# Performance work log

Hardware: AMD Instinct MI355X
Metric: run time of the kernel (lower is better)

Reference implementation:

```python
import jax, jax.numpy as jnp
import numpy as np

N, E = 50000, 800000
IN, HID, H, L, OUT = 128, 64, 2, 2, 40
EPS_SM = 1e-16  # PyG softmax eps
EPS_LN = 1e-5


def setup_inputs() -> dict:
    key = jax.random.key(0)
    ks = jax.random.split(key, 18)
    s = 0.05
    rn = lambda k, sh: jax.random.normal(k, sh, jnp.float32) * s
    return {
        "x": jax.random.normal(ks[0], (N, IN), jnp.float32),
        "edge_index": jax.random.randint(ks[1], (2, E), 0, N, jnp.int64),
        "emb_w": rn(ks[2], (IN, HID)),
        "emb_b": jnp.zeros((HID,), jnp.float32),
        "Wq": rn(ks[3], (L, HID, H * HID)),
        "Wk": rn(ks[4], (L, HID, H * HID)),
        "Wv": rn(ks[5], (L, HID, H * HID)),
        "Wout": rn(ks[6], (L, H * HID, HID)),
        "bout": jnp.zeros((L, HID), jnp.float32),
        "ln_g": jnp.ones((L, HID), jnp.float32),
        "ln_b": jnp.zeros((L, HID), jnp.float32),
        "W1": rn(ks[7], (L, HID, HID)),
        "b1": jnp.zeros((L, HID), jnp.float32),
        "W2": rn(ks[8], (L, HID, HID)),
        "b2": jnp.zeros((L, HID), jnp.float32),
        "out_w": rn(ks[9], (HID, OUT)),
        "out_b": jnp.zeros((OUT,), jnp.float32),
    }


def _layernorm(x, g, b):
    mu = jnp.mean(x, axis=-1, keepdims=True)
    var = jnp.mean(jnp.square(x - mu), axis=-1, keepdims=True)
    return (x - mu) * jax.lax.rsqrt(var + EPS_LN) * g + b


def _gt_layer(h, src, dst, Wq, Wk, Wv, Wout, bout):
    n = h.shape[0]
    Q = (h @ Wq).reshape(n, H, HID)
    K = (h @ Wk).reshape(n, H, HID)
    V = (h @ Wv).reshape(n, H, HID)
    # per-edge gather: q at target i, k/v at source j
    alpha = jnp.sum(Q[dst] * K[src], axis=-1) / np.sqrt(HID)  # [E, H]
    # segment softmax keyed by target node
    amax = jax.ops.segment_max(alpha, dst, num_segments=n)    # [N, H]
    a = jnp.exp(alpha - amax[dst])
    denom = jax.ops.segment_sum(a, dst, num_segments=n)
    a = a / (denom[dst] + EPS_SM)
    msg = V[src] * a[..., None]                               # [E, H, HID]
    aggr = jax.ops.segment_sum(msg, dst, num_segments=n)      # [N, H, HID]
    return aggr.reshape(n, H * HID) @ Wout + bout


def reference(x, edge_index, emb_w, emb_b, Wq, Wk, Wv, Wout, bout,
              ln_g, ln_b, W1, b1, W2, b2, out_w, out_b):
    src, dst = edge_index[0], edge_index[1]
    h = x @ emb_w + emb_b
    for l in range(L):
        res = h
        h = _gt_layer(h, src, dst, Wq[l], Wk[l], Wv[l], Wout[l], bout[l])
        h = _layernorm(h + res, ln_g[l], ln_b[l])
        h = h + (jax.nn.relu(h @ W1[l] + b1[l]) @ W2[l] + b2[l])
    return jax.nn.log_softmax(h @ out_w + out_b, axis=-1)
```

## Files before the change

### kernel.cpp

```cpp
#include <hip/hip_runtime.h>
#include <math.h>

#define DIN 128
#define HID 64
#define BKTSH 7
#define NBKTCAP 512
#define CAPC 2560

typedef _Float16 h2 __attribute__((ext_vector_type(2)));
typedef _Float16 f16x8 __attribute__((ext_vector_type(8)));
typedef float f32x4 __attribute__((ext_vector_type(4)));
typedef float f32x2 __attribute__((ext_vector_type(2)));

__device__ inline unsigned short f2h(float f) {
  return __builtin_bit_cast(unsigned short, (_Float16)f);
}
__device__ inline h2 bch2(unsigned int u) { return __builtin_bit_cast(h2, u); }
__device__ inline unsigned int h2u(h2 x) { return __builtin_bit_cast(unsigned int, x); }
__device__ inline unsigned int pkrtz(float a, float b) {
  return __builtin_bit_cast(unsigned int, __builtin_amdgcn_cvt_pkrtz(a, b));
}
__device__ inline f16x8 bcf16x8(uint4 u) { return __builtin_bit_cast(f16x8, u); }


__global__ __launch_bounds__(256) void k_bktA(const int* __restrict__ dst,
                                              int* __restrict__ bhist,
                                              int nblkA, int E, int nbkt) {
  __shared__ int hist[NBKTCAP];
  int tid = threadIdx.x;
  for (int i = tid; i < nbkt; i += 256) hist[i] = 0;
  __syncthreads();
#pragma unroll
  for (int i = 0; i < 16; ++i) {
    int e = blockIdx.x * 4096 + i * 256 + tid;
    if (e < E) atomicAdd(&hist[dst[e] >> BKTSH], 1);
  }
  __syncthreads();
  for (int i = tid; i < nbkt; i += 256) bhist[i * nblkA + blockIdx.x] = hist[i];
}

__global__ __launch_bounds__(256) void k_bktScan1(int* __restrict__ bhist,
                                                  int* __restrict__ btot,
                                                  int nblkA, int nbkt) {
  int wv = threadIdx.x >> 6, lane = threadIdx.x & 63;
  int b = blockIdx.x * 4 + wv;
  if (b >= nbkt) return;
  int* rowp = bhist + (size_t)b * nblkA;
  int carry = 0;
  for (int base = 0; base < nblkA; base += 64) {
    int i = base + lane;
    int v = (i < nblkA) ? rowp[i] : 0;
    int incl = v;
#pragma unroll
    for (int d = 1; d < 64; d <<= 1) {
      int t = __shfl_up(incl, d, 64);
      if (lane >= d) incl += t;
    }
    if (i < nblkA) rowp[i] = carry + incl - v;
    carry += __shfl(incl, 63, 64);
  }
  if (lane == 0) btot[b] = carry;
}

__global__ __launch_bounds__(512) void k_bktScan2(const int* __restrict__ btot,
                                                  int* __restrict__ bktBase,
                                                  int* __restrict__ rowp,
                                                  int nbkt, int E, int n) {
  __shared__ int sc[512];
  int b = threadIdx.x;
  int s = (b < nbkt) ? btot[b] : 0;
  sc[b] = s;
  __syncthreads();
  for (int d = 1; d < 512; d <<= 1) {
    int v = (b >= d) ? sc[b - d] : 0;
    __syncthreads();
    sc[b] += v;
    __syncthreads();
  }
  if (b < nbkt) bktBase[b] = sc[b] - s;
  if (b == 0) {
    bktBase[nbkt] = E;
    rowp[n] = E;
  }
}

__global__ __launch_bounds__(256) void k_bktB(const int* __restrict__ src,
                                              const int* __restrict__ dst,
                                              const int* __restrict__ bpos,
                                              const int* __restrict__ bktBase,
                                              int2* __restrict__ ebuf,
                                              int nblkA, int E, int nbkt) {
  __shared__ int cur[NBKTCAP];
  int tid = threadIdx.x;
  for (int i = tid; i < nbkt; i += 256)
    cur[i] = bpos[i * nblkA + blockIdx.x] + bktBase[i];
  __syncthreads();
#pragma unroll
  for (int i = 0; i < 16; ++i) {
    int e = blockIdx.x * 4096 + i * 256 + tid;
    if (e < E) {
      int d = dst[e];
      int pos = atomicAdd(&cur[d >> BKTSH], 1);
      ebuf[pos] = make_int2(src[e], d);
    }
  }
}

__global__ __launch_bounds__(256) void k_bktC(const int2* __restrict__ ebuf,
                                              const int* __restrict__ bktBase,
                                              int* __restrict__ rowp,
                                              int* __restrict__ deg,
                                              int* __restrict__ srcs, int n) {
  __shared__ int2 rec[CAPC];
  __shared__ int outv[CAPC];
  __shared__ int hist[128];
  __shared__ int sc[128];
  __shared__ int cur2[128];
  int b = blockIdx.x;
  int tid = threadIdx.x;
  int s0 = bktBase[b], s1 = bktBase[b + 1];
  int cnt = s1 - s0;
  int nodeBase = b << BKTSH;
  if (tid < 128) hist[tid] = 0;
  __syncthreads();
  bool fast = (cnt <= CAPC);
  if (fast) {
    for (int i = tid; i < cnt; i += 256) {
      int2 r = ebuf[s0 + i];
      rec[i] = r;
      atomicAdd(&hist[r.y & 127], 1);
    }
  } else {
    for (int i = tid; i < cnt; i += 256) atomicAdd(&hist[ebuf[s0 + i].y & 127], 1);
  }
  __syncthreads();
  if (tid < 128) sc[tid] = hist[tid];
  __syncthreads();
  for (int d = 1; d < 128; d <<= 1) {
    int v = (tid < 128 && tid >= d) ? sc[tid - d] : 0;
    __syncthreads();
    if (tid < 128) sc[tid] += v;
    __syncthreads();
  }
  if (tid < 128) {
    int excl = sc[tid] - hist[tid];
    int node = nodeBase + tid;
    if (node < n) {
      rowp[node] = s0 + excl;
      deg[node] = hist[tid];
    }
    cur2[tid] = excl;
  }
  __syncthreads();
  if (fast) {
    for (int i = tid; i < cnt; i += 256) {
      int2 r = rec[i];
      int pos = atomicAdd(&cur2[r.y & 127], 1);
      outv[pos] = r.x;
    }
    __syncthreads();
    for (int i = tid; i < cnt; i += 256) srcs[s0 + i] = outv[i];
  } else {
    for (int i = tid; i < cnt; i += 256) {
      int2 r = ebuf[s0 + i];
      int pos = atomicAdd(&cur2[r.y & 127], 1);
      srcs[s0 + pos] = r.x;
    }
  }
}

__global__ __launch_bounds__(256) void k_dhist(const int* __restrict__ cnt,
                                               int* __restrict__ bhist, int n) {
  __shared__ int hist[64];
  int tid = threadIdx.x;
  if (tid < 64) hist[tid] = 0;
  __syncthreads();
  int base = blockIdx.x * 2048 + tid * 8;
#pragma unroll
  for (int i = 0; i < 8; ++i) {
    int idx = base + i;
    if (idx < n) atomicAdd(&hist[min(cnt[idx], 63)], 1);
  }
  __syncthreads();
  if (tid < 64) bhist[blockIdx.x * 64 + tid] = hist[tid];
}

__global__ void k_dscan2(const int* __restrict__ bhist, int* __restrict__ bbase,
                         int nblk) {
  int b = threadIdx.x;
  int tot = 0;
  for (int blk = 0; blk < nblk; ++blk) tot += bhist[blk * 64 + b];
  int incl = tot;
#pragma unroll
  for (int d = 1; d < 64; d <<= 1) {
    int t = __shfl_up(incl, d, 64);
    if (b >= d) incl += t;
  }
  int run = incl - tot;
  for (int blk = 0; blk < nblk; ++blk) {
    bbase[blk * 64 + b] = run;
    run += bhist[blk * 64 + b];
  }
}

__global__ __launch_bounds__(256) void k_dscat2(const int* __restrict__ cnt,
                                                const int* __restrict__ bbase,
                                                int* __restrict__ perm, int n) {
  __shared__ int cur[64];
  int tid = threadIdx.x;
  if (tid < 64) cur[tid] = bbase[blockIdx.x * 64 + tid];
  __syncthreads();
  int base = blockIdx.x * 2048 + tid * 8;
#pragma unroll
  for (int i = 0; i < 8; ++i) {
    int idx = base + i;
    if (idx < n) {
      int pos = atomicAdd(&cur[min(cnt[idx], 63)], 1);
      perm[pos] = idx;
    }
  }
}

__global__ __launch_bounds__(256) void k_wpack(
    const float* __restrict__ Wq, const float* __restrict__ Wk,
    const float* __restrict__ Wv, const float* __restrict__ Wout,
    const float* __restrict__ W1, const float* __restrict__ W2,
    uint4* __restrict__ P) {
  int t = blockIdx.x * 256 + threadIdx.x;
  if (t >= 10240) return;
  int layer = t / 5120;
  int r = t - layer * 5120;
  const float* W;
  int idx, nkk, ld, base;
  float scale = 1.f;
  if (r < 1024) {
    W = Wq + layer * 64 * 128; idx = r; nkk = 2; ld = 128;
    scale = 0.125f * 1.44269504089f; base = 0;
  } else if (r < 2048) {
    W = Wk + layer * 64 * 128; idx = r - 1024; nkk = 2; ld = 128; base = 1024;
  } else if (r < 3072) {
    W = Wv + layer * 64 * 128; idx = r - 2048; nkk = 2; ld = 128; base = 2048;
  } else if (r < 4096) {
    W = Wout + layer * 128 * 64; idx = r - 3072; nkk = 4; ld = 64; base = 3072;
  } else if (r < 4608) {
    W = W1 + layer * 64 * 64; idx = r - 4096; nkk = 2; ld = 64; base = 4096;
  } else {
    W = W2 + layer * 64 * 64; idx = r - 4608; nkk = 2; ld = 64; base = 4608;
  }
  int lane = idx & 63;
  int g = idx >> 6;
  int ct = g / nkk, kk = g - ct * nkk;
  int lc = lane & 15, lg = lane >> 4;
  unsigned short o[8];
#pragma unroll
  for (int i = 0; i < 8; ++i)
    o[i] = f2h(W[(kk * 32 + lg * 8 + i) * ld + ct * 16 + lc] * scale);
  P[layer * 5120 + base + idx] = *(const uint4*)o;
}

__global__ __launch_bounds__(256) void k_wpack2(const float* __restrict__ emb_w,
                                                const float* __restrict__ out_w,
                                                uint4* __restrict__ P) {
  int t = blockIdx.x * 256 + threadIdx.x;
  if (t >= 1408) return;
  int lane, ct, kk, lc, lg;
  unsigned short o[8];
  if (t < 1024) {
    int idx = t;
    lane = idx & 63;
    int g = idx >> 6;
    ct = g >> 2; kk = g & 3;
    lc = lane & 15; lg = lane >> 4;
#pragma unroll
    for (int i = 0; i < 8; ++i)
      o[i] = f2h(emb_w[(kk * 32 + lg * 8 + i) * 64 + ct * 16 + lc]);
    P[10240 + idx] = *(const uint4*)o;
  } else {
    int idx = t - 1024;
    lane = idx & 63;
    int g = idx >> 6;
    ct = g >> 1; kk = g & 1;
    lc = lane & 15; lg = lane >> 4;
    int col = ct * 16 + lc;
#pragma unroll
    for (int i = 0; i < 8; ++i)
      o[i] = (col < 40) ? f2h(out_w[(kk * 32 + lg * 8 + i) * 40 + col]) : (unsigned short)0;
    P[11264 + idx] = *(const uint4*)o;
  }
}

__device__ inline void qkv_mfma(f16x8 af0, f16x8 af1, const uint4* __restrict__ Bq,
                                const uint4* __restrict__ Bk,
                                const uint4* __restrict__ Bv,
                                unsigned short* __restrict__ Qh,
                                unsigned short* __restrict__ KVf8, int nb, int n,
                                int lc, int lg) {
  {
    f32x4 acc[8] = {};
#pragma unroll
    for (int ct = 0; ct < 8; ++ct) {
      acc[ct] = __builtin_amdgcn_mfma_f32_16x16x32_f16(
          af0, bcf16x8(Bq[(ct * 2 + 0) * 64 + lg * 16 + lc]), acc[ct], 0, 0, 0);
      acc[ct] = __builtin_amdgcn_mfma_f32_16x16x32_f16(
          af1, bcf16x8(Bq[(ct * 2 + 1) * 64 + lg * 16 + lc]), acc[ct], 0, 0, 0);
    }
#pragma unroll
    for (int ct = 0; ct < 8; ++ct)
#pragma unroll
      for (int r = 0; r < 4; ++r) {
        int gn = nb + lg * 4 + r;
        if (gn < n) Qh[(size_t)gn * 128 + ct * 16 + lc] = f2h(acc[ct][r]);
      }
  }
#pragma unroll
  for (int ct = 0; ct < 8; ++ct) {
    f32x4 ka = {}, va = {};
    ka = __builtin_amdgcn_mfma_f32_16x16x32_f16(
        af0, bcf16x8(Bk[(ct * 2 + 0) * 64 + lg * 16 + lc]), ka, 0, 0, 0);
    ka = __builtin_amdgcn_mfma_f32_16x16x32_f16(
        af1, bcf16x8(Bk[(ct * 2 + 1) * 64 + lg * 16 + lc]), ka, 0, 0, 0);
    va = __builtin_amdgcn_mfma_f32_16x16x32_f16(
        af0, bcf16x8(Bv[(ct * 2 + 0) * 64 + lg * 16 + lc]), va, 0, 0, 0);
    va = __builtin_amdgcn_mfma_f32_16x16x32_f16(
        af1, bcf16x8(Bv[(ct * 2 + 1) * 64 + lg * 16 + lc]), va, 0, 0, 0);
#pragma unroll
    for (int r = 0; r < 4; ++r) {
      unsigned int pw = (unsigned int)__builtin_amdgcn_cvt_pk_fp8_f32(
          ka[r], va[r], 0, false);
      int gn = nb + lg * 4 + r;
      if (gn < n) KVf8[(size_t)gn * 128 + ct * 16 + lc] = (unsigned short)pw;
    }
  }
}

__global__ __launch_bounds__(256) void k_embqkv(
    const float* __restrict__ x, const uint4* __restrict__ Bemb,
    const float* __restrict__ emb_b, float* __restrict__ h,
    const uint4* __restrict__ Bq, const uint4* __restrict__ Bk,
    const uint4* __restrict__ Bv, unsigned short* __restrict__ Qh,
    unsigned short* __restrict__ KVf8, int n) {
  __shared__ unsigned short red[4][16 * 88];
  int lane = threadIdx.x & 63, wv = threadIdx.x >> 6;
  int nb = (blockIdx.x * 4 + wv) * 16;
  if (nb >= n) return;
  int lc = lane & 15, lg = lane >> 4;

  int arow = (nb + lc < n) ? nb + lc : n - 1;
  const float* xr = x + (size_t)arow * 128;
  f16x8 ax[4];
#pragma unroll
  for (int kk = 0; kk < 4; ++kk) {
    float4 a = *(const float4*)(xr + kk * 32 + lg * 8);
    float4 b = *(const float4*)(xr + kk * 32 + lg * 8 + 4);
    unsigned short o[8] = {f2h(a.x), f2h(a.y), f2h(a.z), f2h(a.w),
                           f2h(b.x), f2h(b.y), f2h(b.z), f2h(b.w)};
    ax[kk] = bcf16x8(*(const uint4*)o);
  }
  f32x4 acc[4] = {};
#pragma unroll
  for (int kk = 0; kk < 4; ++kk)
#pragma unroll
    for (int ct = 0; ct < 4; ++ct)
      acc[ct] = __builtin_amdgcn_mfma_f32_16x16x32_f16(
          ax[kk], bcf16x8(Bemb[(ct * 4 + kk) * 64 + lane]), acc[ct], 0, 0, 0);
#pragma unroll
  for (int ct = 0; ct < 4; ++ct) {
    float bo = emb_b[ct * 16 + lc];
#pragma unroll
    for (int r = 0; r < 4; ++r) {
      float v = acc[ct][r] + bo;
      int gn = nb + lg * 4 + r;
      if (gn < n) h[(size_t)gn * 64 + ct * 16 + lc] = v;
      red[wv][(lg * 4 + r) * 88 + ct * 16 + lc] = f2h(v);
    }
  }
  f16x8 af0 = bcf16x8(*(const uint4*)&red[wv][lc * 88 + lg * 8]);
  f16x8 af1 = bcf16x8(*(const uint4*)&red[wv][lc * 88 + 32 + lg * 8]);
  qkv_mfma(af0, af1, Bq, Bk, Bv, Qh, KVf8, nb, n, lc, lg);
}

__global__ __launch_bounds__(256) void k_attn(
    const unsigned short* __restrict__ Qh, const unsigned short* __restrict__ KVf8,
    const int* __restrict__ row, const int* __restrict__ srcs,
    const int* __restrict__ perm,
    unsigned short* __restrict__ aggrh, int n) {
  int lane = threadIdx.x & 63;
  int w = threadIdx.x >> 6;
  int idx = blockIdx.x * 4 + w;
  if (idx >= n) return;
  int node = perm[idx];
  int sl = lane & 15, gi = lane >> 4;

  uint4 qr = *(const uint4*)(Qh + (size_t)node * 128 + sl * 8);
  h2 qh0 = bch2(qr.x), qh1 = bch2(qr.y), qh2 = bch2(qr.z), qh3 = bch2(qr.w);
  float q0 = (float)qh0[0], q1 = (float)qh0[1], q2 = (float)qh1[0], q3 = (float)qh1[1];
  float q4 = (float)qh2[0], q5 = (float)qh2[1], q6 = (float)qh3[0], q7 = (float)qh3[1];

  int rs = row[node], re = row[node + 1];
  int deg = re - rs;
  float den = 0.f;
  float a0 = 0.f, a1 = 0.f, a2 = 0.f, a3 = 0.f;
  float a4 = 0.f, a5 = 0.f, a6 = 0.f, a7 = 0.f;

  if (deg > 0) {
    int iters = (deg + 3) >> 2;
    uint4 Kb[4];
    int sxb[4];
#pragma unroll
    for (int s = 0; s < 4; ++s) {
      if (s < iters) {
        int ei = rs + s * 4 + gi;
        int sx = (ei < re) ? srcs[ei] : srcs[rs];
        Kb[s] = *(const uint4*)(KVf8 + (size_t)sx * 128 + sl * 8);
      }
      int ei2 = rs + (s + 4) * 4 + gi;
      sxb[s] = (ei2 < re) ? srcs[ei2] : srcs[rs];
    }
    for (int it = 0; it < iters; it += 4) {
#pragma unroll
      for (int s = 0; s < 4; ++s) {
        int cit = it + s;
        if (cit < iters) {
          uint4 Wd = Kb[s];
          if (cit + 4 < iters) {
            Kb[s] = *(const uint4*)(KVf8 + (size_t)sxb[s] * 128 + sl * 8);
          }
          {
            int ei3 = rs + (cit + 8) * 4 + gi;
            sxb[s] = (ei3 < re) ? srcs[ei3] : srcs[rs];
          }
          f32x2 p0 = __builtin_amdgcn_cvt_pk_f32_fp8(Wd.x, false);
          f32x2 p1 = __builtin_amdgcn_cvt_pk_f32_fp8(Wd.x, true);
          f32x2 p2 = __builtin_amdgcn_cvt_pk_f32_fp8(Wd.y, false);
          f32x2 p3 = __builtin_amdgcn_cvt_pk_f32_fp8(Wd.y, true);
          f32x2 p4 = __builtin_amdgcn_cvt_pk_f32_fp8(Wd.z, false);
          f32x2 p5 = __builtin_amdgcn_cvt_pk_f32_fp8(Wd.z, true);
          f32x2 p6 = __builtin_amdgcn_cvt_pk_f32_fp8(Wd.w, false);
          f32x2 p7 = __builtin_amdgcn_cvt_pk_f32_fp8(Wd.w, true);
          float sc = q0 * p0.x + q1 * p1.x + q2 * p2.x + q3 * p3.x +
                     q4 * p4.x + q5 * p5.x + q6 * p6.x + q7 * p7.x;
          sc += __shfl_xor(sc, 1, 64);
          sc += __shfl_xor(sc, 2, 64);
          sc += __shfl_xor(sc, 4, 64);
          bool ev = (rs + cit * 4 + gi) < re;
          float wgt = ev ? __builtin_amdgcn_exp2f(sc) : 0.f;
          den += wgt;
          a0 += wgt * p0.y;
          a1 += wgt * p1.y;
          a2 += wgt * p2.y;
          a3 += wgt * p3.y;
          a4 += wgt * p4.y;
          a5 += wgt * p5.y;
          a6 += wgt * p6.y;
          a7 += wgt * p7.y;
        }
      }
    }
  }
#pragma unroll
  for (int d = 16; d < 64; d <<= 1) {
    den += __shfl_xor(den, d, 64);
    a0 += __shfl_xor(a0, d, 64);
    a1 += __shfl_xor(a1, d, 64);
    a2 += __shfl_xor(a2, d, 64);
    a3 += __shfl_xor(a3, d, 64);
    a4 += __shfl_xor(a4, d, 64);
    a5 += __shfl_xor(a5, d, 64);
    a6 += __shfl_xor(a6, d, 64);
    a7 += __shfl_xor(a7, d, 64);
  }
  float inv = fminf(1.f / (den + 1e-16f), 60000.f);
  if (lane < 16) {
    uint4 o;
    o.x = pkrtz(a0 * inv, a1 * inv);
    o.y = pkrtz(a2 * inv, a3 * inv);
    o.z = pkrtz(a4 * inv, a5 * inv);
    o.w = pkrtz(a6 * inv, a7 * inv);
    *(uint4*)(aggrh + (size_t)node * 128 + sl * 8) = o;
  }
}

template <int MODE>
__global__ __launch_bounds__(256) void k_post(
    const unsigned short* __restrict__ aggrh, float* __restrict__ h,
    const uint4* __restrict__ Bout, const float* __restrict__ bout,
    const float* __restrict__ lng, const float* __restrict__ lnb,
    const uint4* __restrict__ B1, const float* __restrict__ b1,
    const uint4* __restrict__ B2, const float* __restrict__ b2,
    const uint4* __restrict__ BqN, const uint4* __restrict__ BkN,
    const uint4* __restrict__ BvN, unsigned short* __restrict__ Qh,
    unsigned short* __restrict__ KVf8,
    const uint4* __restrict__ Bo, const float* __restrict__ out_b,
    float* __restrict__ out, int n) {
  __shared__ unsigned short red[4][16 * 88];
  int lane = threadIdx.x & 63, wv = threadIdx.x >> 6;
  int nb = (blockIdx.x * 4 + wv) * 16;
  if (nb >= n) return;
  int lc = lane & 15, lg = lane >> 4;

  f32x4 acc[4] = {};
  const uint4* arow_p = (const uint4*)(aggrh + (size_t)(nb + lc) * 128);
#pragma unroll
  for (int kk = 0; kk < 4; ++kk) {
    f16x8 af = bcf16x8(arow_p[kk * 4 + lg]);
#pragma unroll
    for (int ct = 0; ct < 4; ++ct)
      acc[ct] = __builtin_amdgcn_mfma_f32_16x16x32_f16(
          af, bcf16x8(Bout[(ct * 4 + kk) * 64 + lane]), acc[ct], 0, 0, 0);
  }

  float x[4][4], hl[4][4];
#pragma unroll
  for (int ct = 0; ct < 4; ++ct) {
    float bo = bout[ct * 16 + lc];
#pragma unroll
    for (int r = 0; r < 4; ++r)
      x[r][ct] = acc[ct][r] + bo + h[(size_t)(nb + lg * 4 + r) * 64 + ct * 16 + lc];
  }
  float g[4], bb[4];
#pragma unroll
  for (int ct = 0; ct < 4; ++ct) {
    g[ct] = lng[ct * 16 + lc];
    bb[ct] = lnb[ct * 16 + lc];
  }
#pragma unroll
  for (int r = 0; r < 4; ++r) {
    float s = x[r][0] + x[r][1] + x[r][2] + x[r][3];
    s += __shfl_xor(s, 1, 64);
    s += __shfl_xor(s, 2, 64);
    s += __shfl_xor(s, 4, 64);
    s += __shfl_xor(s, 8, 64);
    float mu = s * (1.f / 64.f);
    float s2 = 0.f;
#pragma unroll
    for (int ct = 0; ct < 4; ++ct) {
      float xc = x[r][ct] - mu;
      s2 += xc * xc;
    }
    s2 += __shfl_xor(s2, 1, 64);
    s2 += __shfl_xor(s2, 2, 64);
    s2 += __shfl_xor(s2, 4, 64);
    s2 += __shfl_xor(s2, 8, 64);
    float inv = rsqrtf(s2 * (1.f / 64.f) + 1e-5f);
#pragma unroll
    for (int ct = 0; ct < 4; ++ct) {
      hl[r][ct] = (x[r][ct] - mu) * inv * g[ct] + bb[ct];
      red[wv][(lg * 4 + r) * 88 + ct * 16 + lc] = f2h(hl[r][ct]);
    }
  }

  f32x4 acc2[4] = {};
#pragma unroll
  for (int kk = 0; kk < 2; ++kk) {
    f16x8 af = bcf16x8(*(const uint4*)&red[wv][lc * 88 + kk * 32 + lg * 8]);
#pragma unroll
    for (int ct = 0; ct < 4; ++ct)
      acc2[ct] = __builtin_amdgcn_mfma_f32_16x16x32_f16(
          af, bcf16x8(B1[(ct * 2 + kk) * 64 + lane]), acc2[ct], 0, 0, 0);
  }
#pragma unroll
  for (int ct = 0; ct < 4; ++ct) {
    float b1c = b1[ct * 16 + lc];
#pragma unroll
    for (int r = 0; r < 4; ++r)
      red[wv][(lg * 4 + r) * 88 + ct * 16 + lc] = f2h(fmaxf(acc2[ct][r] + b1c, 0.f));
  }

  f32x4 acc3[4] = {};
#pragma unroll
  for (int kk = 0; kk < 2; ++kk) {
    f16x8 af = bcf16x8(*(const uint4*)&red[wv][lc * 88 + kk * 32 + lg * 8]);
#pragma unroll
    for (int ct = 0; ct < 4; ++ct)
      acc3[ct] = __builtin_amdgcn_mfma_f32_16x16x32_f16(
          af, bcf16x8(B2[(ct * 2 + kk) * 64 + lane]), acc3[ct], 0, 0, 0);
  }
#pragma unroll
  for (int ct = 0; ct < 4; ++ct) {
    float b2c = b2[ct * 16 + lc];
#pragma unroll
    for (int r = 0; r < 4; ++r) {
      float v = hl[r][ct] + acc3[ct][r] + b2c;
      int gn = nb + lg * 4 + r;
      if (MODE == 0 && gn < n) h[(size_t)gn * 64 + ct * 16 + lc] = v;
      red[wv][(lg * 4 + r) * 88 + ct * 16 + lc] = f2h(v);
    }
  }

  if (MODE == 0) {
    f16x8 af0 = bcf16x8(*(const uint4*)&red[wv][lc * 88 + lg * 8]);
    f16x8 af1 = bcf16x8(*(const uint4*)&red[wv][lc * 88 + 32 + lg * 8]);
    qkv_mfma(af0, af1, BqN, BkN, BvN, Qh, KVf8, nb, n, lc, lg);
  } else {
    f32x4 lg4[3] = {};
#pragma unroll
    for (int kk = 0; kk < 2; ++kk) {
      f16x8 af = bcf16x8(*(const uint4*)&red[wv][lc * 88 + kk * 32 + lg * 8]);
#pragma unroll
      for (int ct = 0; ct < 3; ++ct)
        lg4[ct] = __builtin_amdgcn_mfma_f32_16x16x32_f16(
            af, bcf16x8(Bo[(ct * 2 + kk) * 64 + lane]), lg4[ct], 0, 0, 0);
    }
    float ob0 = out_b[lc], ob1 = out_b[16 + lc];
    float ob2 = (lc < 8) ? out_b[32 + lc] : 0.f;
#pragma unroll
    for (int r = 0; r < 4; ++r) {
      float l0 = lg4[0][r] + ob0;
      float l1 = lg4[1][r] + ob1;
      float l2 = (lc < 8) ? (lg4[2][r] + ob2) : -3.0e38f;
      float m = fmaxf(fmaxf(l0, l1), l2);
      m = fmaxf(m, __shfl_xor(m, 1, 64));
      m = fmaxf(m, __shfl_xor(m, 2, 64));
      m = fmaxf(m, __shfl_xor(m, 4, 64));
      m = fmaxf(m, __shfl_xor(m, 8, 64));
      float e = __expf(l0 - m) + __expf(l1 - m) + ((lc < 8) ? __expf(l2 - m) : 0.f);
      e += __shfl_xor(e, 1, 64);
      e += __shfl_xor(e, 2, 64);
      e += __shfl_xor(e, 4, 64);
      e += __shfl_xor(e, 8, 64);
      float ls = m + logf(e);
      int gn = nb + lg * 4 + r;
      if (gn < n) {
        out[(size_t)gn * 40 + lc] = l0 - ls;
        out[(size_t)gn * 40 + 16 + lc] = l1 - ls;
        if (lc < 8) out[(size_t)gn * 40 + 32 + lc] = l2 - ls;
      }
    }
  }
}

extern "C" void kernel_launch(void* const* d_in, const int* in_sizes, int n_in,
                              void* d_out, int out_size, void* d_ws, size_t ws_size,
                              hipStream_t stream) {
  const float* x     = (const float*)d_in[0];
  const int*   ei    = (const int*)d_in[1];
  const float* emb_w = (const float*)d_in[2];
  const float* emb_b = (const float*)d_in[3];
  const float* Wq    = (const float*)d_in[4];
  const float* Wk    = (const float*)d_in[5];
  const float* Wv    = (const float*)d_in[6];
  const float* Wout  = (const float*)d_in[7];
  const float* bout  = (const float*)d_in[8];
  const float* ln_g  = (const float*)d_in[9];
  const float* ln_b  = (const float*)d_in[10];
  const float* W1    = (const float*)d_in[11];
  const float* b1    = (const float*)d_in[12];
  const float* W2    = (const float*)d_in[13];
  const float* b2    = (const float*)d_in[14];
  const float* out_w = (const float*)d_in[15];
  const float* out_b = (const float*)d_in[16];
  float* out = (float*)d_out;

  const int n = in_sizes[0] / DIN;
  const int E = in_sizes[1] / 2;

  char* ws = (char*)d_ws;
  size_t off = 0;
  auto alloc = [&](size_t bytes) {
    void* p = ws + off;
    off = (off + bytes + 255) & ~(size_t)255;
    return p;
  };
  float* h              = (float*)alloc((size_t)n * 64 * 4);
  unsigned short* Qh    = (unsigned short*)alloc((size_t)n * 128 * 2);
  unsigned short* KVf8  = (unsigned short*)alloc((size_t)n * 128 * 2);
  unsigned short* aggrh = (unsigned short*)alloc((size_t)n * 128 * 2);
  int* rowp             = (int*)alloc((size_t)(n + 1) * 4);
  int* srcs             = (int*)alloc((size_t)E * 4);
  int* deg              = (int*)alloc((size_t)n * 4);
  int* perm             = (int*)alloc((size_t)n * 4);
  uint4* WP             = (uint4*)alloc((size_t)11648 * 16);
  int nblkA             = (E + 4095) / 4096;
  int nbkt              = (n + 127) >> BKTSH;
  int* bhist2           = (int*)alloc((size_t)NBKTCAP * nblkA * 4);
  int* btot             = (int*)alloc((size_t)NBKTCAP * 4);
  int* bktBase          = (int*)alloc((size_t)(NBKTCAP + 1) * 4);
  int2* ebuf            = (int2*)alloc((size_t)E * 8);
  int nScanBlk          = (n + 2047) / 2048;
  int* bhist            = (int*)alloc((size_t)nScanBlk * 64 * 4);
  int* bbase            = (int*)alloc((size_t)nScanBlk * 64 * 4);

  const int* src = ei;
  const int* dst = ei + E;

  k_bktA<<<nblkA, 256, 0, stream>>>(dst, bhist2, nblkA, E, nbkt);
  k_bktScan1<<<(nbkt + 3) / 4, 256, 0, stream>>>(bhist2, btot, nblkA, nbkt);
  k_bktScan2<<<1, 512, 0, stream>>>(btot, bktBase, rowp, nbkt, E, n);
  k_bktB<<<nblkA, 256, 0, stream>>>(src, dst, bhist2, bktBase, ebuf, nblkA, E, nbkt);
  k_bktC<<<nbkt, 256, 0, stream>>>(ebuf, bktBase, rowp, deg, srcs, n);
  k_dhist<<<nScanBlk, 256, 0, stream>>>(deg, bhist, n);
  k_dscan2<<<1, 64, 0, stream>>>(bhist, bbase, nScanBlk);
  k_dscat2<<<nScanBlk, 256, 0, stream>>>(deg, bbase, perm, n);

  k_wpack<<<40, 256, 0, stream>>>(Wq, Wk, Wv, Wout, W1, W2, WP);
  k_wpack2<<<6, 256, 0, stream>>>(emb_w, out_w, WP);

  const uint4* L0 = WP;
  const uint4* L1 = WP + 5120;
  const uint4* Bemb = WP + 10240;
  const uint4* Bo = WP + 11264;

  k_embqkv<<<(n + 63) / 64, 256, 0, stream>>>(x, Bemb, emb_b, h, L0, L0 + 1024,
                                              L0 + 2048, Qh, KVf8, n);

  k_attn<<<(n + 3) / 4, 256, 0, stream>>>(Qh, KVf8, rowp, srcs, perm, aggrh, n);
  k_post<0><<<(n + 63) / 64, 256, 0, stream>>>(
      aggrh, h, L0 + 3072, bout, ln_g, ln_b, L0 + 4096, b1, L0 + 4608, b2,
      L1, L1 + 1024, L1 + 2048, Qh, KVf8, nullptr, nullptr, nullptr, n);

  k_attn<<<(n + 3) / 4, 256, 0, stream>>>(Qh, KVf8, rowp, srcs, perm, aggrh, n);
  k_post<1><<<(n + 63) / 64, 256, 0, stream>>>(
      aggrh, h, L1 + 3072, bout + 64, ln_g + 64, ln_b + 64, L1 + 4096, b1 + 64,
      L1 + 4608, b2 + 64, nullptr, nullptr, nullptr, nullptr, nullptr,
      Bo, out_b, out, n);
}
```

Before: 203.1 us.

## Split K/V into separate fp8 planes with permuted channel layout, drop degree sort

K and V are now stored as separate packed fp8 rows (4 channels per lane, interleaved per head) instead of K/V pairs in one 16-bit word. Q and the Wout weight rows are permuted to match, and the attention loop uses packed f32x2 math. The degree-sort permutation kernels (histogram, scan, scatter) are removed, so attention now walks nodes in natural order. This saves three launches and a perm lookup, but gives up the load balancing that degree-sorted scheduling provided.

```diff
diff --git a/kernel.cpp b/kernel.cpp
--- a/kernel.cpp
+++ b/kernel.cpp
@@ -16,7 +16,6 @@
   return __builtin_bit_cast(unsigned short, (_Float16)f);
 }
 __device__ inline h2 bch2(unsigned int u) { return __builtin_bit_cast(h2, u); }
-__device__ inline unsigned int h2u(h2 x) { return __builtin_bit_cast(unsigned int, x); }
 __device__ inline unsigned int pkrtz(float a, float b) {
   return __builtin_bit_cast(unsigned int, __builtin_amdgcn_cvt_pkrtz(a, b));
 }
@@ -109,7 +108,6 @@
 __global__ __launch_bounds__(256) void k_bktC(const int2* __restrict__ ebuf,
                                               const int* __restrict__ bktBase,
                                               int* __restrict__ rowp,
-                                              int* __restrict__ deg,
                                               int* __restrict__ srcs, int n) {
   __shared__ int2 rec[CAPC];
   __shared__ int outv[CAPC];
@@ -145,10 +143,7 @@
   if (tid < 128) {
     int excl = sc[tid] - hist[tid];
     int node = nodeBase + tid;
-    if (node < n) {
-      rowp[node] = s0 + excl;
-      deg[node] = hist[tid];
-    }
+    if (node < n) rowp[node] = s0 + excl;
     cur2[tid] = excl;
   }
   __syncthreads();
@@ -165,58 +160,6 @@
       int2 r = ebuf[s0 + i];
       int pos = atomicAdd(&cur2[r.y & 127], 1);
       srcs[s0 + pos] = r.x;
-    }
-  }
-}
-
-__global__ __launch_bounds__(256) void k_dhist(const int* __restrict__ cnt,
-                                               int* __restrict__ bhist, int n) {
-  __shared__ int hist[64];
-  int tid = threadIdx.x;
-  if (tid < 64) hist[tid] = 0;
-  __syncthreads();
-  int base = blockIdx.x * 2048 + tid * 8;
-#pragma unroll
-  for (int i = 0; i < 8; ++i) {
-    int idx = base + i;
-    if (idx < n) atomicAdd(&hist[min(cnt[idx], 63)], 1);
-  }
-  __syncthreads();
-  if (tid < 64) bhist[blockIdx.x * 64 + tid] = hist[tid];
-}
-
-__global__ void k_dscan2(const int* __restrict__ bhist, int* __restrict__ bbase,
-                         int nblk) {
-  int b = threadIdx.x;
-  int tot = 0;
-  for (int blk = 0; blk < nblk; ++blk) tot += bhist[blk * 64 + b];
-  int incl = tot;
-#pragma unroll
-  for (int d = 1; d < 64; d <<= 1) {
-    int t = __shfl_up(incl, d, 64);
-    if (b >= d) incl += t;
-  }
-  int run = incl - tot;
-  for (int blk = 0; blk < nblk; ++blk) {
-    bbase[blk * 64 + b] = run;
-    run += bhist[blk * 64 + b];
-  }
-}
-
-__global__ __launch_bounds__(256) void k_dscat2(const int* __restrict__ cnt,
-                                                const int* __restrict__ bbase,
-                                                int* __restrict__ perm, int n) {
-  __shared__ int cur[64];
-  int tid = threadIdx.x;
-  if (tid < 64) cur[tid] = bbase[blockIdx.x * 64 + tid];
-  __syncthreads();
-  int base = blockIdx.x * 2048 + tid * 8;
-#pragma unroll
-  for (int i = 0; i < 8; ++i) {
-    int idx = base + i;
-    if (idx < n) {
-      int pos = atomicAdd(&cur[min(cnt[idx], 63)], 1);
-      perm[pos] = idx;
     }
   }
 }
@@ -233,6 +176,7 @@
   const float* W;
   int idx, nkk, ld, base;
   float scale = 1.f;
+  bool permk = false;
   if (r < 1024) {
     W = Wq + layer * 64 * 128; idx = r; nkk = 2; ld = 128;
     scale = 0.125f * 1.44269504089f; base = 0;
@@ -242,6 +186,7 @@
     W = Wv + layer * 64 * 128; idx = r - 2048; nkk = 2; ld = 128; base = 2048;
   } else if (r < 4096) {
     W = Wout + layer * 128 * 64; idx = r - 3072; nkk = 4; ld = 64; base = 3072;
+    permk = true;
   } else if (r < 4608) {
     W = W1 + layer * 64 * 64; idx = r - 4096; nkk = 2; ld = 64; base = 4096;
   } else {
@@ -253,8 +198,14 @@
   int lc = lane & 15, lg = lane >> 4;
   unsigned short o[8];
 #pragma unroll
-  for (int i = 0; i < 8; ++i)
-    o[i] = f2h(W[(kk * 32 + lg * 8 + i) * ld + ct * 16 + lc] * scale);
+  for (int i = 0; i < 8; ++i) {
+    int rr = kk * 32 + lg * 8 + i;
+    if (permk) {
+      int bb = rr & 63;
+      rr = (rr & 64) + (bb & 3) * 16 + (bb >> 2);
+    }
+    o[i] = f2h(W[rr * ld + ct * 16 + lc] * scale);
+  }
   P[layer * 5120 + base + idx] = *(const uint4*)o;
 }
 
@@ -293,7 +244,7 @@
                                 const uint4* __restrict__ Bk,
                                 const uint4* __restrict__ Bv,
                                 unsigned short* __restrict__ Qh,
-                                unsigned short* __restrict__ KVf8, int nb, int n,
+                                unsigned char* __restrict__ KVf8, int nb, int n,
                                 int lc, int lg) {
   {
     f32x4 acc[8] = {};
@@ -305,30 +256,46 @@
           af1, bcf16x8(Bq[(ct * 2 + 1) * 64 + lg * 16 + lc]), acc[ct], 0, 0, 0);
     }
 #pragma unroll
-    for (int ct = 0; ct < 8; ++ct)
+    for (int ct = 0; ct < 8; ++ct) {
+      int pos = (ct >> 2) * 64 + lc * 4 + (ct & 3);
 #pragma unroll
       for (int r = 0; r < 4; ++r) {
         int gn = nb + lg * 4 + r;
-        if (gn < n) Qh[(size_t)gn * 128 + ct * 16 + lc] = f2h(acc[ct][r]);
+        if (gn < n) Qh[(size_t)gn * 128 + pos] = f2h(acc[ct][r]);
       }
-  }
-#pragma unroll
-  for (int ct = 0; ct < 8; ++ct) {
-    f32x4 ka = {}, va = {};
-    ka = __builtin_amdgcn_mfma_f32_16x16x32_f16(
-        af0, bcf16x8(Bk[(ct * 2 + 0) * 64 + lg * 16 + lc]), ka, 0, 0, 0);
-    ka = __builtin_amdgcn_mfma_f32_16x16x32_f16(
-        af1, bcf16x8(Bk[(ct * 2 + 1) * 64 + lg * 16 + lc]), ka, 0, 0, 0);
-    va = __builtin_amdgcn_mfma_f32_16x16x32_f16(
-        af0, bcf16x8(Bv[(ct * 2 + 0) * 64 + lg * 16 + lc]), va, 0, 0, 0);
-    va = __builtin_amdgcn_mfma_f32_16x16x32_f16(
-        af1, bcf16x8(Bv[(ct * 2 + 1) * 64 + lg * 16 + lc]), va, 0, 0, 0);
+    }
+  }
+#pragma unroll
+  for (int head = 0; head < 2; ++head) {
+    f32x4 ka[4], va[4];
+#pragma unroll
+    for (int c4 = 0; c4 < 4; ++c4) {
+      int ct = head * 4 + c4;
+      f32x4 kz = {}, vz = {};
+      kz = __builtin_amdgcn_mfma_f32_16x16x32_f16(
+          af0, bcf16x8(Bk[(ct * 2 + 0) * 64 + lg * 16 + lc]), kz, 0, 0, 0);
+      kz = __builtin_amdgcn_mfma_f32_16x16x32_f16(
+          af1, bcf16x8(Bk[(ct * 2 + 1) * 64 + lg * 16 + lc]), kz, 0, 0, 0);
+      vz = __builtin_amdgcn_mfma_f32_16x16x32_f16(
+          af0, bcf16x8(Bv[(ct * 2 + 0) * 64 + lg * 16 + lc]), vz, 0, 0, 0);
+      vz = __builtin_amdgcn_mfma_f32_16x16x32_f16(
+          af1, bcf16x8(Bv[(ct * 2 + 1) * 64 + lg * 16 + lc]), vz, 0, 0, 0);
+      ka[c4] = kz;
+      va[c4] = vz;
+    }
 #pragma unroll
     for (int r = 0; r < 4; ++r) {
-      unsigned int pw = (unsigned int)__builtin_amdgcn_cvt_pk_fp8_f32(
-          ka[r], va[r], 0, false);
+      int kw = __builtin_amdgcn_cvt_pk_fp8_f32(ka[0][r], ka[1][r], 0, false);
+      kw = __builtin_amdgcn_cvt_pk_fp8_f32(ka[2][r], ka[3][r], kw, true);
+      int vw = __builtin_amdgcn_cvt_pk_fp8_f32(va[0][r], va[1][r], 0, false);
+      vw = __builtin_amdgcn_cvt_pk_fp8_f32(va[2][r], va[3][r], vw, true);
       int gn = nb + lg * 4 + r;
-      if (gn < n) KVf8[(size_t)gn * 128 + ct * 16 + lc] = (unsigned short)pw;
+      if (gn < n) {
+        *(unsigned int*)(KVf8 + (size_t)gn * 256 + head * 64 + lc * 4) =
+            (unsigned int)kw;
+        *(unsigned int*)(KVf8 + (size_t)gn * 256 + 128 + head * 64 + lc * 4) =
+            (unsigned int)vw;
+      }
     }
   }
 }
@@ -338,7 +305,7 @@
     const float* __restrict__ emb_b, float* __restrict__ h,
     const uint4* __restrict__ Bq, const uint4* __restrict__ Bk,
     const uint4* __restrict__ Bv, unsigned short* __restrict__ Qh,
-    unsigned short* __restrict__ KVf8, int n) {
+    unsigned char* __restrict__ KVf8, int n) {
   __shared__ unsigned short red[4][16 * 88];
   int lane = threadIdx.x & 63, wv = threadIdx.x >> 6;
   int nb = (blockIdx.x * 4 + wv) * 16;
@@ -380,38 +347,39 @@
 }
 
 __global__ __launch_bounds__(256) void k_attn(
-    const unsigned short* __restrict__ Qh, const unsigned short* __restrict__ KVf8,
+    const unsigned short* __restrict__ Qh, const unsigned char* __restrict__ KVf8,
     const int* __restrict__ row, const int* __restrict__ srcs,
-    const int* __restrict__ perm,
     unsigned short* __restrict__ aggrh, int n) {
   int lane = threadIdx.x & 63;
   int w = threadIdx.x >> 6;
-  int idx = blockIdx.x * 4 + w;
-  if (idx >= n) return;
-  int node = perm[idx];
+  int node = blockIdx.x * 4 + w;
+  if (node >= n) return;
   int sl = lane & 15, gi = lane >> 4;
 
   uint4 qr = *(const uint4*)(Qh + (size_t)node * 128 + sl * 8);
   h2 qh0 = bch2(qr.x), qh1 = bch2(qr.y), qh2 = bch2(qr.z), qh3 = bch2(qr.w);
-  float q0 = (float)qh0[0], q1 = (float)qh0[1], q2 = (float)qh1[0], q3 = (float)qh1[1];
-  float q4 = (float)qh2[0], q5 = (float)qh2[1], q6 = (float)qh3[0], q7 = (float)qh3[1];
+  f32x2 q01 = {(float)qh0[0], (float)qh0[1]};
+  f32x2 q23 = {(float)qh1[0], (float)qh1[1]};
+  f32x2 q45 = {(float)qh2[0], (float)qh2[1]};
+  f32x2 q67 = {(float)qh3[0], (float)qh3[1]};
 
   int rs = row[node], re = row[node + 1];
   int deg = re - rs;
   float den = 0.f;
-  float a0 = 0.f, a1 = 0.f, a2 = 0.f, a3 = 0.f;
-  float a4 = 0.f, a5 = 0.f, a6 = 0.f, a7 = 0.f;
+  f32x2 av0 = {0, 0}, av1 = {0, 0}, av2 = {0, 0}, av3 = {0, 0};
 
   if (deg > 0) {
     int iters = (deg + 3) >> 2;
-    uint4 Kb[4];
+    uint2 Kb[4], Vb[4];
     int sxb[4];
 #pragma unroll
     for (int s = 0; s < 4; ++s) {
       if (s < iters) {
         int ei = rs + s * 4 + gi;
         int sx = (ei < re) ? srcs[ei] : srcs[rs];
-        Kb[s] = *(const uint4*)(KVf8 + (size_t)sx * 128 + sl * 8);
+        const unsigned char* rp = KVf8 + (size_t)sx * 256;
+        Kb[s] = *(const uint2*)(rp + sl * 8);
+        Vb[s] = *(const uint2*)(rp + 128 + sl * 8);
       }
       int ei2 = rs + (s + 4) * 4 + gi;
       sxb[s] = (ei2 < re) ? srcs[ei2] : srcs[rs];
@@ -421,38 +389,32 @@
       for (int s = 0; s < 4; ++s) {
         int cit = it + s;
         if (cit < iters) {
-          uint4 Wd = Kb[s];
+          uint2 Kd = Kb[s], Vd = Vb[s];
           if (cit + 4 < iters) {
-            Kb[s] = *(const uint4*)(KVf8 + (size_t)sxb[s] * 128 + sl * 8);
+            const unsigned char* rp = KVf8 + (size_t)sxb[s] * 256;
+            Kb[s] = *(const uint2*)(rp + sl * 8);
+            Vb[s] = *(const uint2*)(rp + 128 + sl * 8);
           }
           {
             int ei3 = rs + (cit + 8) * 4 + gi;
             sxb[s] = (ei3 < re) ? srcs[ei3] : srcs[rs];
           }
-          f32x2 p0 = __builtin_amdgcn_cvt_pk_f32_fp8(Wd.x, false);
-          f32x2 p1 = __builtin_amdgcn_cvt_pk_f32_fp8(Wd.x, true);
-          f32x2 p2 = __builtin_amdgcn_cvt_pk_f32_fp8(Wd.y, false);
-          f32x2 p3 = __builtin_amdgcn_cvt_pk_f32_fp8(Wd.y, true);
-          f32x2 p4 = __builtin_amdgcn_cvt_pk_f32_fp8(Wd.z, false);
-          f32x2 p5 = __builtin_amdgcn_cvt_pk_f32_fp8(Wd.z, true);
-          f32x2 p6 = __builtin_amdgcn_cvt_pk_f32_fp8(Wd.w, false);
-          f32x2 p7 = __builtin_amdgcn_cvt_pk_f32_fp8(Wd.w, true);
-          float sc = q0 * p0.x + q1 * p1.x + q2 * p2.x + q3 * p3.x +
-                     q4 * p4.x + q5 * p5.x + q6 * p6.x + q7 * p7.x;
+          f32x2 s2 = __builtin_amdgcn_cvt_pk_f32_fp8(Kd.x, false) * q01;
+          s2 += __builtin_amdgcn_cvt_pk_f32_fp8(Kd.x, true) * q23;
+          s2 += __builtin_amdgcn_cvt_pk_f32_fp8(Kd.y, false) * q45;
+          s2 += __builtin_amdgcn_cvt_pk_f32_fp8(Kd.y, true) * q67;
+          float sc = s2.x + s2.y;
           sc += __shfl_xor(sc, 1, 64);
           sc += __shfl_xor(sc, 2, 64);
           sc += __shfl_xor(sc, 4, 64);
           bool ev = (rs + cit * 4 + gi) < re;
           float wgt = ev ? __builtin_amdgcn_exp2f(sc) : 0.f;
           den += wgt;
-          a0 += wgt * p0.y;
-          a1 += wgt * p1.y;
-          a2 += wgt * p2.y;
-          a3 += wgt * p3.y;
-          a4 += wgt * p4.y;
-          a5 += wgt * p5.y;
-          a6 += wgt * p6.y;
-          a7 += wgt * p7.y;
+          f32x2 w2 = {wgt, wgt};
+          av0 += w2 * __builtin_amdgcn_cvt_pk_f32_fp8(Vd.x, false);
+          av1 += w2 * __builtin_amdgcn_cvt_pk_f32_fp8(Vd.x, true);
+          av2 += w2 * __builtin_amdgcn_cvt_pk_f32_fp8(Vd.y, false);
+          av3 += w2 * __builtin_amdgcn_cvt_pk_f32_fp8(Vd.y, true);
         }
       }
     }
@@ -460,22 +422,22 @@
 #pragma unroll
   for (int d = 16; d < 64; d <<= 1) {
     den += __shfl_xor(den, d, 64);
-    a0 += __shfl_xor(a0, d, 64);
-    a1 += __shfl_xor(a1, d, 64);
-    a2 += __shfl_xor(a2, d, 64);
-    a3 += __shfl_xor(a3, d, 64);
-    a4 += __shfl_xor(a4, d, 64);
-    a5 += __shfl_xor(a5, d, 64);
-    a6 += __shfl_xor(a6, d, 64);
-    a7 += __shfl_xor(a7, d, 64);
+    av0.x += __shfl_xor(av0.x, d, 64);
+    av0.y += __shfl_xor(av0.y, d, 64);
+    av1.x += __shfl_xor(av1.x, d, 64);
+    av1.y += __shfl_xor(av1.y, d, 64);
+    av2.x += __shfl_xor(av2.x, d, 64);
+    av2.y += __shfl_xor(av2.y, d, 64);
+    av3.x += __shfl_xor(av3.x, d, 64);
+    av3.y += __shfl_xor(av3.y, d, 64);
   }
   float inv = fminf(1.f / (den + 1e-16f), 60000.f);
   if (lane < 16) {
     uint4 o;
-    o.x = pkrtz(a0 * inv, a1 * inv);
-    o.y = pkrtz(a2 * inv, a3 * inv);
-    o.z = pkrtz(a4 * inv, a5 * inv);
-    o.w = pkrtz(a6 * inv, a7 * inv);
+    o.x = pkrtz(av0.x * inv, av0.y * inv);
+    o.y = pkrtz(av1.x * inv, av1.y * inv);
+    o.z = pkrtz(av2.x * inv, av2.y * inv);
+    o.w = pkrtz(av3.x * inv, av3.y * inv);
     *(uint4*)(aggrh + (size_t)node * 128 + sl * 8) = o;
   }
 }
@@ -489,7 +451,7 @@
     const uint4* __restrict__ B2, const float* __restrict__ b2,
     const uint4* __restrict__ BqN, const uint4* __restrict__ BkN,
     const uint4* __restrict__ BvN, unsigned short* __restrict__ Qh,
-    unsigned short* __restrict__ KVf8,
+    unsigned char* __restrict__ KVf8,
     const uint4* __restrict__ Bo, const float* __restrict__ out_b,
     float* __restrict__ out, int n) {
   __shared__ unsigned short red[4][16 * 88];
@@ -663,12 +625,10 @@
   };
   float* h              = (float*)alloc((size_t)n * 64 * 4);
   unsigned short* Qh    = (unsigned short*)alloc((size_t)n * 128 * 2);
-  unsigned short* KVf8  = (unsigned short*)alloc((size_t)n * 128 * 2);
+  unsigned char* KVf8   = (unsigned char*)alloc((size_t)n * 256);
   unsigned short* aggrh = (unsigned short*)alloc((size_t)n * 128 * 2);
   int* rowp             = (int*)alloc((size_t)(n + 1) * 4);
   int* srcs             = (int*)alloc((size_t)E * 4);
-  int* deg              = (int*)alloc((size_t)n * 4);
-  int* perm             = (int*)alloc((size_t)n * 4);
   uint4* WP             = (uint4*)alloc((size_t)11648 * 16);
   int nblkA             = (E + 4095) / 4096;
   int nbkt              = (n + 127) >> BKTSH;
@@ -676,9 +636,6 @@
   int* btot             = (int*)alloc((size_t)NBKTCAP * 4);
   int* bktBase          = (int*)alloc((size_t)(NBKTCAP + 1) * 4);
   int2* ebuf            = (int2*)alloc((size_t)E * 8);
-  int nScanBlk          = (n + 2047) / 2048;
-  int* bhist            = (int*)alloc((size_t)nScanBlk * 64 * 4);
-  int* bbase            = (int*)alloc((size_t)nScanBlk * 64 * 4);
 
   const int* src = ei;
   const int* dst = ei + E;
@@ -687,10 +644,7 @@
   k_bktScan1<<<(nbkt + 3) / 4, 256, 0, stream>>>(bhist2, btot, nblkA, nbkt);
   k_bktScan2<<<1, 512, 0, stream>>>(btot, bktBase, rowp, nbkt, E, n);
   k_bktB<<<nblkA, 256, 0, stream>>>(src, dst, bhist2, bktBase, ebuf, nblkA, E, nbkt);
-  k_bktC<<<nbkt, 256, 0, stream>>>(ebuf, bktBase, rowp, deg, srcs, n);
-  k_dhist<<<nScanBlk, 256, 0, stream>>>(deg, bhist, n);
-  k_dscan2<<<1, 64, 0, stream>>>(bhist, bbase, nScanBlk);
-  k_dscat2<<<nScanBlk, 256, 0, stream>>>(deg, bbase, perm, n);
+  k_bktC<<<nbkt, 256, 0, stream>>>(ebuf, bktBase, rowp, srcs, n);
 
   k_wpack<<<40, 256, 0, stream>>>(Wq, Wk, Wv, Wout, W1, W2, WP);
   k_wpack2<<<6, 256, 0, stream>>>(emb_w, out_w, WP);
@@ -703,12 +657,12 @@
   k_embqkv<<<(n + 63) / 64, 256, 0, stream>>>(x, Bemb, emb_b, h, L0, L0 + 1024,
                                               L0 + 2048, Qh, KVf8, n);
 
-  k_attn<<<(n + 3) / 4, 256, 0, stream>>>(Qh, KVf8, rowp, srcs, perm, aggrh, n);
+  k_attn<<<(n + 3) / 4, 256, 0, stream>>>(Qh, KVf8, rowp, srcs, aggrh, n);
   k_post<0><<<(n + 63) / 64, 256, 0, stream>>>(
       aggrh, h, L0 + 3072, bout, ln_g, ln_b, L0 + 4096, b1, L0 + 4608, b2,
       L1, L1 + 1024, L1 + 2048, Qh, KVf8, nullptr, nullptr, nullptr, n);
 
-  k_attn<<<(n + 3) / 4, 256, 0, stream>>>(Qh, KVf8, rowp, srcs, perm, aggrh, n);
+  k_attn<<<(n + 3) / 4, 256, 0, stream>>>(Qh, KVf8, rowp, srcs, aggrh, n);
   k_post<1><<<(n + 63) / 64, 256, 0, stream>>>(
       aggrh, h, L1 + 3072, bout + 64, ln_g + 64, ln_b + 64, L1 + 4096, b1 + 64,
       L1 + 4608, b2 + 64, nullptr, nullptr, nullptr, nullptr, nullptr,
```

Measured after the change: 186.2 us. -8.3%, faster.
